# Kernel optimization log

Hardware: AMD Instinct MI355X
Metric: run time of the kernel (lower is better)

Reference implementation:

```python
import jax, jax.numpy as jnp
import numpy as np

B, S, D, EXP = 2, 2048, 128, 16
N = D * EXP  # state_dim = 2048


def setup_inputs() -> dict:
    key = jax.random.key(0)
    ks = jax.random.split(key, 11)
    s_in = 1.0 / np.sqrt(D)   # torch Linear default init bound for dim->N layers
    s_out = 1.0 / np.sqrt(N)  # for out_proj (N->dim)
    x = jax.random.normal(ks[0], (B, S, D), dtype=jnp.float32)
    W_B = jax.random.uniform(ks[1], (N, D), jnp.float32, -s_in, s_in)
    b_B = jax.random.uniform(ks[2], (N,), jnp.float32, -s_in, s_in)
    W_C = jax.random.uniform(ks[3], (N, D), jnp.float32, -s_in, s_in)
    b_C = jax.random.uniform(ks[4], (N,), jnp.float32, -s_in, s_in)
    W_dt = jax.random.uniform(ks[5], (N, D), jnp.float32, -s_in, s_in)
    b_dt = jax.random.uniform(ks[6], (N,), jnp.float32, -s_in, s_in)
    A_log = jnp.log(jax.random.uniform(ks[7], (N,), jnp.float32) * 0.5 + 0.5)
    W_out = jax.random.uniform(ks[8], (D, N), jnp.float32, -s_out, s_out)
    b_out = jax.random.uniform(ks[9], (D,), jnp.float32, -s_out, s_out)
    return {"x": x, "W_B": W_B, "b_B": b_B, "W_C": W_C, "b_C": b_C,
            "W_dt": W_dt, "b_dt": b_dt, "A_log": A_log,
            "W_out": W_out, "b_out": b_out}


def reference(x, W_B, b_B, W_C, b_C, W_dt, b_dt, A_log, W_out, b_out):
    # Featurizer projections: [B,S,D] -> [B,S,N]
    B_feat = jnp.einsum('bsd,nd->bsn', x, W_B) + b_B
    C_feat = jnp.einsum('bsd,nd->bsn', x, W_C) + b_C
    dt = jax.nn.softplus(jnp.einsum('bsd,nd->bsn', x, W_dt) + b_dt)
    A = -jnp.exp(A_log)                # [N]
    A_bar = jnp.exp(dt * A)            # [B,S,N]
    B_bar = dt * B_feat                # [B,S,N]

    # Sequential diagonal scan: h_t = A_t * h_{t-1} + B_t ; y_t = C_t * h_t
    def step(h, abc):
        a_t, b_t, c_t = abc            # each [B,N]
        h = a_t * h + b_t
        return h, c_t * h

    h0 = jnp.zeros((x.shape[0], N), dtype=x.dtype)
    xs = (jnp.swapaxes(A_bar, 0, 1),   # [S,B,N]
          jnp.swapaxes(B_bar, 0, 1),
          jnp.swapaxes(C_feat, 0, 1))
    _, ys = jax.lax.scan(step, h0, xs)  # ys: [S,B,N]
    y = jnp.swapaxes(ys, 0, 1)          # [B,S,N]
    return jnp.einsum('bsn,dn->bsd', y, W_out) + b_out
```

## Files before the change

### kernel.cpp

```cpp
#include <hip/hip_runtime.h>


#define BB 2
#define SS 2048
#define DDIM 128
#define NDIM 2048
#define TT (BB*SS)
#define NTILE (TT/16)

typedef short short8 __attribute__((ext_vector_type(8)));
typedef float floatx4 __attribute__((ext_vector_type(4)));

__device__ __forceinline__ unsigned short f2b(float f){
  unsigned u = __float_as_uint(f);
  u += 0x7FFFu + ((u >> 16) & 1u);
  return (unsigned short)(u >> 16);
}
__device__ __forceinline__ float softplus_f(float v){
  return v > 15.f ? v : __logf(1.f + __expf(v));
}
__device__ __forceinline__ void pack8(const float* __restrict__ s,
                                      unsigned short* __restrict__ d){
  floatx4 v0 = *(const floatx4*)s;
  floatx4 v1 = *(const floatx4*)(s + 4);
  short8 r;
  r[0]=(short)f2b(v0[0]); r[1]=(short)f2b(v0[1]); r[2]=(short)f2b(v0[2]); r[3]=(short)f2b(v0[3]);
  r[4]=(short)f2b(v1[0]); r[5]=(short)f2b(v1[1]); r[6]=(short)f2b(v1[2]); r[7]=(short)f2b(v1[3]);
  *(short8*)d = r;
}

__global__ void prep_kernel(const float* __restrict__ x,
                            const float* __restrict__ W_B,
                            const float* __restrict__ W_C,
                            const float* __restrict__ W_dt,
                            const float* __restrict__ A_log,
                            const float* __restrict__ W_out,
                            unsigned short* __restrict__ xp,
                            unsigned short* __restrict__ Wp3,
                            unsigned short* __restrict__ Wop,
                            float* __restrict__ Aval,
                            unsigned long long* __restrict__ Sbuf){
  const int gid = blockIdx.x * blockDim.x + threadIdx.x;
  if (gid < 32768) Sbuf[gid] = 0ull;
  if (gid < 2048) Aval[gid] = -__expf(A_log[gid]);
  if (gid < 65536){
    int g = gid, tile = g >> 8, kk = (g >> 6) & 3, lane = g & 63;
    int q = lane >> 4, m = lane & 15;
    pack8(x + (size_t)(tile*16 + m)*DDIM + kk*32 + q*8, xp + (size_t)g*8);
  }
  if (gid < 98304){
    int mat = gid >> 15, g = gid & 32767;
    const float* W = (mat == 0) ? W_B : (mat == 1 ? W_dt : W_C);
    int tile = g >> 8, kk = (g >> 6) & 3, lane = g & 63;
    int q = lane >> 4, m = lane & 15;
    pack8(W + (size_t)(tile*16 + m)*DDIM + kk*32 + q*8,
          Wp3 + (size_t)mat*262144 + (size_t)g*8);
  }
  if (gid < 32768){
    int g = gid, tile = g >> 12, kk = (g >> 6) & 63, lane = g & 63;
    int q = lane >> 4, m = lane & 15;
    pack8(W_out + (size_t)(tile*16 + m)*NDIM + kk*32 + q*8, Wop + (size_t)g*8);
  }
}

__global__ __launch_bounds__(256, 2) void projscan_kernel(
    const unsigned short* __restrict__ xp,
    const unsigned short* __restrict__ Wp3,
    const float* __restrict__ b_B,
    const float* __restrict__ b_dt,
    const float* __restrict__ b_C,
    const float* __restrict__ Aval,
    unsigned long long* __restrict__ Sbuf,
    unsigned short* __restrict__ ybp){
  __shared__ unsigned short sW[3*4096];
  __shared__ unsigned short sYT[4][16*40];
  __shared__ float sPw[4][32], sHw[4][32];
  __shared__ float sIw[4][32];
  const int tid  = threadIdx.x;
  const int lane = tid & 63;
  const int wv   = tid >> 6;
  const int m    = lane & 15;
  const int q    = lane >> 4;
  const int p    = blockIdx.y * 16 + blockIdx.x;
  const int xcd  = p & 7;
  const int slot = p >> 3;
  const int rr   = slot & 15;
  const int j    = slot >> 4;
  const int row  = xcd*16 + rr;
  const int by   = row >> 1;
  const int bx   = (row & 1)*8 + j;
  const int n0   = by*32;

  for (int i = tid; i < 1536; i += 256){
    int mat = i >> 9, rem = i & 511;
    *(short8*)(sW + mat*4096 + rem*8) =
        *(const short8*)(Wp3 + (size_t)mat*262144 + (size_t)by*4096 + rem*8);
  }
  __syncthreads();

  float bBv[2], bDv[2], bCv[2], Avv[2];
#pragma unroll
  for (int nt = 0; nt < 2; ++nt){
    const int n = n0 + nt*16 + m;
    bBv[nt] = b_B[n]; bDv[nt] = b_dt[n]; bCv[nt] = b_C[n]; Avv[nt] = Aval[n];
  }

  unsigned ypk[4][2][2], cpk[4][2][2];
  float pe_t[4][2], he_t[4][2];
  float pa_run[2] = {1.f, 1.f}, ha_run[2] = {0.f, 0.f};

#pragma unroll
  for (int i = 0; i < 4; ++i){
    const int tile = bx*16 + wv*4 + i;
    short8 xf[4];
#pragma unroll
    for (int kk = 0; kk < 4; ++kk)
      xf[kk] = *(const short8*)(xp + (size_t)tile*2048 + kk*512 + lane*8);

    floatx4 acc[3][2];
#pragma unroll
    for (int mat = 0; mat < 3; ++mat)
#pragma unroll
      for (int nt = 0; nt < 2; ++nt)
        acc[mat][nt] = (floatx4){0.f,0.f,0.f,0.f};
#pragma unroll
    for (int nt = 0; nt < 2; ++nt)
#pragma unroll
      for (int kk = 0; kk < 4; ++kk){
        short8 wB = *(const short8*)(sW +         nt*2048 + kk*512 + lane*8);
        short8 wD = *(const short8*)(sW + 4096 +  nt*2048 + kk*512 + lane*8);
        short8 wC = *(const short8*)(sW + 8192 +  nt*2048 + kk*512 + lane*8);
        acc[0][nt] = __builtin_amdgcn_mfma_f32_16x16x32_bf16(xf[kk], wB, acc[0][nt], 0, 0, 0);
        acc[1][nt] = __builtin_amdgcn_mfma_f32_16x16x32_bf16(xf[kk], wD, acc[1][nt], 0, 0, 0);
        acc[2][nt] = __builtin_amdgcn_mfma_f32_16x16x32_bf16(xf[kk], wC, acc[2][nt], 0, 0, 0);
      }

#pragma unroll
    for (int nt = 0; nt < 2; ++nt){
      float Ar[4], Br[4], Cc[4];
#pragma unroll
      for (int r = 0; r < 4; ++r){
        float dtv = softplus_f(acc[1][nt][r] + bDv[nt]);
        Ar[r] = __expf(dtv * Avv[nt]);
        Br[r] = dtv * (acc[0][nt][r] + bBv[nt]);
        Cc[r] = acc[2][nt][r] + bCv[nt];
      }
      float P = Ar[0], H = Br[0];
#pragma unroll
      for (int r = 1; r < 4; ++r){ H = Ar[r]*H + Br[r]; P *= Ar[r]; }
      float pp = __shfl(P, (lane - 16) & 63, 64);
      float hh = __shfl(H, (lane - 16) & 63, 64);
      if (q >= 1){ H = P*hh + H; P *= pp; }
      pp = __shfl(P, (lane - 32) & 63, 64);
      hh = __shfl(H, (lane - 32) & 63, 64);
      if (q >= 2){ H = P*hh + H; P *= pp; }
      float pe = __shfl(P, (lane - 16) & 63, 64);
      float he = __shfl(H, (lane - 16) & 63, 64);
      if (q == 0){ pe = 1.f; he = 0.f; }
      float pb = __shfl(P, m + 48, 64);
      float hb = __shfl(H, m + 48, 64);

      float h = he, pa = pe;
      unsigned short yr[4], cr[4];
#pragma unroll
      for (int r = 0; r < 4; ++r){
        h = Ar[r]*h + Br[r];
        pa *= Ar[r];
        yr[r] = f2b(Cc[r]*h);
        cr[r] = f2b(Cc[r]*pa);
      }
      ypk[i][nt][0] = (unsigned)yr[0] | ((unsigned)yr[1] << 16);
      ypk[i][nt][1] = (unsigned)yr[2] | ((unsigned)yr[3] << 16);
      cpk[i][nt][0] = (unsigned)cr[0] | ((unsigned)cr[1] << 16);
      cpk[i][nt][1] = (unsigned)cr[2] | ((unsigned)cr[3] << 16);

      pe_t[i][nt] = pa_run[nt];
      he_t[i][nt] = ha_run[nt];
      ha_run[nt] = pb*ha_run[nt] + hb;
      pa_run[nt] *= pb;
    }
  }
  if (q == 0){
#pragma unroll
    for (int nt = 0; nt < 2; ++nt){
      sPw[wv][nt*16 + m] = pa_run[nt];
      sHw[wv][nt*16 + m] = ha_run[nt];
    }
  }
  __syncthreads();

  if (tid < 32){
    float Pw[4], Hw[4];
#pragma unroll
    for (int w2 = 0; w2 < 4; ++w2){ Pw[w2] = sPw[w2][tid]; Hw[w2] = sHw[w2][tid]; }
    float pb = 1.f, hb = 0.f;
#pragma unroll
    for (int w2 = 0; w2 < 4; ++w2){ hb = Pw[w2]*hb + Hw[w2]; pb *= Pw[w2]; }
    float pbc = fmaxf(pb, 1e-30f);
    __hip_atomic_store(Sbuf + (size_t)(by*16 + bx)*32 + tid,
        ((unsigned long long)__float_as_uint(pbc) << 32) |
         (unsigned long long)__float_as_uint(hb),
        __ATOMIC_RELAXED, __HIP_MEMORY_SCOPE_AGENT);
    float S = 0.f;
    const int cnt = bx & 7;
    if (cnt){
      const int j0 = bx & ~7;
      unsigned long long v0=0,v1=0,v2=0,v3=0,v4=0,v5=0,v6=0;
      unsigned got = 0;
      const unsigned all = (1u << cnt) - 1u;
      const unsigned long long* base = Sbuf + (size_t)(by*16 + j0)*32 + tid;
      for (;;){
#define LOOKBACK(J, V)                                                          \
        if (J < cnt && !(got & (1u << J))){                                     \
          unsigned long long a = __hip_atomic_load(base + (size_t)J*32,         \
              __ATOMIC_RELAXED, __HIP_MEMORY_SCOPE_AGENT);                      \
          if ((unsigned)(a >> 32) != 0u){ V = a; got |= 1u << J; }              \
        }
        LOOKBACK(0, v0) LOOKBACK(1, v1) LOOKBACK(2, v2) LOOKBACK(3, v3)
        LOOKBACK(4, v4) LOOKBACK(5, v5) LOOKBACK(6, v6)
#undef LOOKBACK
        if (got == all) break;
        __builtin_amdgcn_s_sleep(1);
      }
#define COMPOSE(J, V)                                                           \
      if (J < cnt) S = __uint_as_float((unsigned)(V >> 32))*S +                 \
                       __uint_as_float((unsigned)V);
      COMPOSE(0, v0) COMPOSE(1, v1) COMPOSE(2, v2) COMPOSE(3, v3)
      COMPOSE(4, v4) COMPOSE(5, v5) COMPOSE(6, v6)
#undef COMPOSE
    }
    float s = S;
#pragma unroll
    for (int w2 = 0; w2 < 4; ++w2){
      sIw[w2][tid] = s;
      s = Pw[w2]*s + Hw[w2];
    }
  }
  __syncthreads();

  float iw[2];
#pragma unroll
  for (int nt = 0; nt < 2; ++nt) iw[nt] = sIw[wv][nt*16 + m];
#pragma unroll
  for (int i = 0; i < 4; ++i){
    const int tile = bx*16 + wv*4 + i;
#pragma unroll
    for (int nt = 0; nt < 2; ++nt){
      float it = pe_t[i][nt]*iw[nt] + he_t[i][nt];
#pragma unroll
      for (int j2 = 0; j2 < 2; ++j2){
        unsigned yp = ypk[i][nt][j2], cp = cpk[i][nt][j2];
        float y0 = __uint_as_float(yp << 16);
        float y1 = __uint_as_float(yp & 0xffff0000u);
        float c0 = __uint_as_float(cp << 16);
        float c1 = __uint_as_float(cp & 0xffff0000u);
        sYT[wv][(q*4 + j2*2 + 0)*40 + nt*16 + m] = f2b(y0 + c0*it);
        sYT[wv][(q*4 + j2*2 + 1)*40 + nt*16 + m] = f2b(y1 + c1*it);
      }
    }
    short8 yv = *(const short8*)&sYT[wv][m*40 + q*8];
    *(short8*)(ybp + (size_t)tile*32768 + (size_t)by*512 + (size_t)lane*8) = yv;
  }
}

__global__ void outproj_kernel(const unsigned short* __restrict__ ybp,
                               const unsigned short* __restrict__ Wop,
                               const float* __restrict__ b_out,
                               float* __restrict__ out){
  __shared__ float red[4*2048];
  const int tid  = threadIdx.x;
  const int lane = tid & 63;
  const int wv   = tid >> 6;
  const int m    = lane & 15;
  const int q    = lane >> 4;
  const int tile = blockIdx.x;

  floatx4 acc[8];
#pragma unroll
  for (int dt = 0; dt < 8; ++dt) acc[dt] = (floatx4){0.f,0.f,0.f,0.f};

  const unsigned short* aP = ybp + (size_t)tile*32768 + lane*8;
  const unsigned short* bP = Wop + (size_t)lane*8;
#pragma unroll 4
  for (int kk = wv*16; kk < wv*16 + 16; ++kk){
    short8 af = *(const short8*)(aP + (size_t)kk*512);
#pragma unroll
    for (int dt = 0; dt < 8; ++dt){
      short8 bf = *(const short8*)(bP + (size_t)dt*32768 + (size_t)kk*512);
      acc[dt] = __builtin_amdgcn_mfma_f32_16x16x32_bf16(af, bf, acc[dt], 0, 0, 0);
    }
  }
#pragma unroll
  for (int dt = 0; dt < 8; ++dt)
#pragma unroll
    for (int r = 0; r < 4; ++r)
      red[wv*2048 + (q*4 + r)*128 + dt*16 + m] = acc[dt][r];
  __syncthreads();
#pragma unroll
  for (int i = 0; i < 8; ++i){
    int idx = i*256 + tid;
    float s = red[idx] + red[2048 + idx] + red[4096 + idx] + red[6144 + idx];
    int tl = idx >> 7, d = idx & 127;
    out[(size_t)(tile*16 + tl)*DDIM + d] = s + b_out[d];
  }
}

extern "C" void kernel_launch(void* const* d_in, const int* in_sizes, int n_in,
                              void* d_out, int out_size, void* d_ws, size_t ws_size,
                              hipStream_t stream) {
  const float* x     = (const float*)d_in[0];
  const float* W_B   = (const float*)d_in[1];
  const float* b_B   = (const float*)d_in[2];
  const float* W_C   = (const float*)d_in[3];
  const float* b_C   = (const float*)d_in[4];
  const float* W_dt  = (const float*)d_in[5];
  const float* b_dt  = (const float*)d_in[6];
  const float* A_log = (const float*)d_in[7];
  const float* W_out = (const float*)d_in[8];
  const float* b_out = (const float*)d_in[9];
  float* out = (float*)d_out;

  char* w = (char*)d_ws;
  unsigned short* xp    = (unsigned short*)(w + 0x0000000);
  unsigned short* Wp3   = (unsigned short*)(w + 0x0100000);
  unsigned short* Wop   = (unsigned short*)(w + 0x0280000);
  float*          Aval  = (float*)         (w + 0x0300000);
  unsigned short* ybp   = (unsigned short*)(w + 0x0310000);
  unsigned long long* Sbuf = (unsigned long long*)(w + 0x1310000);

  prep_kernel<<<384, 256, 0, stream>>>(
      x, W_B, W_C, W_dt, A_log, W_out, xp, Wp3, Wop, Aval, Sbuf);

  projscan_kernel<<<dim3(16, 64), 256, 0, stream>>>(
      xp, Wp3, b_B, b_dt, b_C, Aval, Sbuf, ybp);

  outproj_kernel<<<NTILE, 256, 0, stream>>>(ybp, Wop, b_out, out);
}
```

Before: 115.5 us.

## Recompute projections after lookback instead of holding scan state in registers

The first pass of the projection-scan kernel now computes only the B and dt projections, enough to form block carries. After the decoupled lookback it recomputes all three projections and the local scan, applies the incoming carry directly, and packs outputs with a hardware bf16 convert instruction. This removes the large per-thread arrays of packed y/c values that were held across the lookback, cutting register pressure at the cost of repeating the MFMA and transcendental work. The change also lengthens the lookback sleep with a backoff, and doubles outproj to 512 threads so each wave handles half as many k-slices, with a larger shared reduction.

Result: slower. 118.3 us (+2.4%).

```diff
diff --git a/kernel.cpp b/kernel.cpp
--- a/kernel.cpp
+++ b/kernel.cpp
@@ -15,6 +15,11 @@
   unsigned u = __float_as_uint(f);
   u += 0x7FFFu + ((u >> 16) & 1u);
   return (unsigned short)(u >> 16);
+}
+__device__ __forceinline__ unsigned cvt_pk_bf16(float lo, float hi){
+  unsigned r;
+  asm("v_cvt_pk_bf16_f32 %0, %1, %2" : "=v"(r) : "v"(lo), "v"(hi));
+  return r;
 }
 __device__ __forceinline__ float softplus_f(float v){
   return v > 15.f ? v : __logf(1.f + __expf(v));
@@ -73,7 +78,7 @@
     unsigned long long* __restrict__ Sbuf,
     unsigned short* __restrict__ ybp){
   __shared__ unsigned short sW[3*4096];
-  __shared__ unsigned short sYT[4][16*40];
+  __shared__ unsigned short sYT[4][640];
   __shared__ float sPw[4][32], sHw[4][32];
   __shared__ float sIw[4][32];
   const int tid  = threadIdx.x;
@@ -105,10 +110,7 @@
     bBv[nt] = b_B[n]; bDv[nt] = b_dt[n]; bCv[nt] = b_C[n]; Avv[nt] = Aval[n];
   }
 
-  unsigned ypk[4][2][2], cpk[4][2][2];
-  float pe_t[4][2], he_t[4][2];
   float pa_run[2] = {1.f, 1.f}, ha_run[2] = {0.f, 0.f};
-
 #pragma unroll
   for (int i = 0; i < 4; ++i){
     const int tile = bx*16 + wv*4 + i;
@@ -117,65 +119,45 @@
     for (int kk = 0; kk < 4; ++kk)
       xf[kk] = *(const short8*)(xp + (size_t)tile*2048 + kk*512 + lane*8);
 
-    floatx4 acc[3][2];
-#pragma unroll
-    for (int mat = 0; mat < 3; ++mat)
-#pragma unroll
-      for (int nt = 0; nt < 2; ++nt)
-        acc[mat][nt] = (floatx4){0.f,0.f,0.f,0.f};
+    floatx4 aB[2], aD[2];
+#pragma unroll
+    for (int nt = 0; nt < 2; ++nt){
+      aB[nt] = (floatx4){0.f,0.f,0.f,0.f};
+      aD[nt] = (floatx4){0.f,0.f,0.f,0.f};
+    }
 #pragma unroll
     for (int nt = 0; nt < 2; ++nt)
 #pragma unroll
       for (int kk = 0; kk < 4; ++kk){
         short8 wB = *(const short8*)(sW +         nt*2048 + kk*512 + lane*8);
         short8 wD = *(const short8*)(sW + 4096 +  nt*2048 + kk*512 + lane*8);
-        short8 wC = *(const short8*)(sW + 8192 +  nt*2048 + kk*512 + lane*8);
-        acc[0][nt] = __builtin_amdgcn_mfma_f32_16x16x32_bf16(xf[kk], wB, acc[0][nt], 0, 0, 0);
-        acc[1][nt] = __builtin_amdgcn_mfma_f32_16x16x32_bf16(xf[kk], wD, acc[1][nt], 0, 0, 0);
-        acc[2][nt] = __builtin_amdgcn_mfma_f32_16x16x32_bf16(xf[kk], wC, acc[2][nt], 0, 0, 0);
+        aB[nt] = __builtin_amdgcn_mfma_f32_16x16x32_bf16(xf[kk], wB, aB[nt], 0, 0, 0);
+        aD[nt] = __builtin_amdgcn_mfma_f32_16x16x32_bf16(xf[kk], wD, aD[nt], 0, 0, 0);
       }
 
 #pragma unroll
     for (int nt = 0; nt < 2; ++nt){
-      float Ar[4], Br[4], Cc[4];
-#pragma unroll
-      for (int r = 0; r < 4; ++r){
-        float dtv = softplus_f(acc[1][nt][r] + bDv[nt]);
-        Ar[r] = __expf(dtv * Avv[nt]);
-        Br[r] = dtv * (acc[0][nt][r] + bBv[nt]);
-        Cc[r] = acc[2][nt][r] + bCv[nt];
-      }
-      float P = Ar[0], H = Br[0];
-#pragma unroll
-      for (int r = 1; r < 4; ++r){ H = Ar[r]*H + Br[r]; P *= Ar[r]; }
+      float P, H;
+      {
+        float Ar[4], Br[4];
+#pragma unroll
+        for (int r = 0; r < 4; ++r){
+          float dtv = softplus_f(aD[nt][r] + bDv[nt]);
+          Ar[r] = __expf(dtv * Avv[nt]);
+          Br[r] = dtv * (aB[nt][r] + bBv[nt]);
+        }
+        P = Ar[0]; H = Br[0];
+#pragma unroll
+        for (int r = 1; r < 4; ++r){ H = Ar[r]*H + Br[r]; P *= Ar[r]; }
+      }
       float pp = __shfl(P, (lane - 16) & 63, 64);
       float hh = __shfl(H, (lane - 16) & 63, 64);
       if (q >= 1){ H = P*hh + H; P *= pp; }
       pp = __shfl(P, (lane - 32) & 63, 64);
       hh = __shfl(H, (lane - 32) & 63, 64);
       if (q >= 2){ H = P*hh + H; P *= pp; }
-      float pe = __shfl(P, (lane - 16) & 63, 64);
-      float he = __shfl(H, (lane - 16) & 63, 64);
-      if (q == 0){ pe = 1.f; he = 0.f; }
       float pb = __shfl(P, m + 48, 64);
       float hb = __shfl(H, m + 48, 64);
-
-      float h = he, pa = pe;
-      unsigned short yr[4], cr[4];
-#pragma unroll
-      for (int r = 0; r < 4; ++r){
-        h = Ar[r]*h + Br[r];
-        pa *= Ar[r];
-        yr[r] = f2b(Cc[r]*h);
-        cr[r] = f2b(Cc[r]*pa);
-      }
-      ypk[i][nt][0] = (unsigned)yr[0] | ((unsigned)yr[1] << 16);
-      ypk[i][nt][1] = (unsigned)yr[2] | ((unsigned)yr[3] << 16);
-      cpk[i][nt][0] = (unsigned)cr[0] | ((unsigned)cr[1] << 16);
-      cpk[i][nt][1] = (unsigned)cr[2] | ((unsigned)cr[3] << 16);
-
-      pe_t[i][nt] = pa_run[nt];
-      he_t[i][nt] = ha_run[nt];
       ha_run[nt] = pb*ha_run[nt] + hb;
       pa_run[nt] *= pb;
     }
@@ -207,6 +189,7 @@
       const int j0 = bx & ~7;
       unsigned long long v0=0,v1=0,v2=0,v3=0,v4=0,v5=0,v6=0;
       unsigned got = 0;
+      int spin = 0;
       const unsigned all = (1u << cnt) - 1u;
       const unsigned long long* base = Sbuf + (size_t)(by*16 + j0)*32 + tid;
       for (;;){
@@ -220,7 +203,9 @@
         LOOKBACK(4, v4) LOOKBACK(5, v5) LOOKBACK(6, v6)
 #undef LOOKBACK
         if (got == all) break;
-        __builtin_amdgcn_s_sleep(1);
+        if (spin < 4) __builtin_amdgcn_s_sleep(2);
+        else          __builtin_amdgcn_s_sleep(8);
+        ++spin;
       }
 #define COMPOSE(J, V)                                                           \
       if (J < cnt) S = __uint_as_float((unsigned)(V >> 32))*S +                 \
@@ -238,36 +223,88 @@
   }
   __syncthreads();
 
-  float iw[2];
-#pragma unroll
-  for (int nt = 0; nt < 2; ++nt) iw[nt] = sIw[wv][nt*16 + m];
+  float it_run[2];
+#pragma unroll
+  for (int nt = 0; nt < 2; ++nt) it_run[nt] = sIw[wv][nt*16 + m];
+
 #pragma unroll
   for (int i = 0; i < 4; ++i){
     const int tile = bx*16 + wv*4 + i;
+    short8 xf[4];
+#pragma unroll
+    for (int kk = 0; kk < 4; ++kk)
+      xf[kk] = *(const short8*)(xp + (size_t)tile*2048 + kk*512 + lane*8);
+
+    floatx4 acc[3][2];
+#pragma unroll
+    for (int mat = 0; mat < 3; ++mat)
+#pragma unroll
+      for (int nt = 0; nt < 2; ++nt)
+        acc[mat][nt] = (floatx4){0.f,0.f,0.f,0.f};
+#pragma unroll
+    for (int nt = 0; nt < 2; ++nt)
+#pragma unroll
+      for (int kk = 0; kk < 4; ++kk){
+        short8 wB = *(const short8*)(sW +         nt*2048 + kk*512 + lane*8);
+        short8 wD = *(const short8*)(sW + 4096 +  nt*2048 + kk*512 + lane*8);
+        short8 wC = *(const short8*)(sW + 8192 +  nt*2048 + kk*512 + lane*8);
+        acc[0][nt] = __builtin_amdgcn_mfma_f32_16x16x32_bf16(xf[kk], wB, acc[0][nt], 0, 0, 0);
+        acc[1][nt] = __builtin_amdgcn_mfma_f32_16x16x32_bf16(xf[kk], wD, acc[1][nt], 0, 0, 0);
+        acc[2][nt] = __builtin_amdgcn_mfma_f32_16x16x32_bf16(xf[kk], wC, acc[2][nt], 0, 0, 0);
+      }
+
 #pragma unroll
     for (int nt = 0; nt < 2; ++nt){
-      float it = pe_t[i][nt]*iw[nt] + he_t[i][nt];
-#pragma unroll
-      for (int j2 = 0; j2 < 2; ++j2){
-        unsigned yp = ypk[i][nt][j2], cp = cpk[i][nt][j2];
-        float y0 = __uint_as_float(yp << 16);
-        float y1 = __uint_as_float(yp & 0xffff0000u);
-        float c0 = __uint_as_float(cp << 16);
-        float c1 = __uint_as_float(cp & 0xffff0000u);
-        sYT[wv][(q*4 + j2*2 + 0)*40 + nt*16 + m] = f2b(y0 + c0*it);
-        sYT[wv][(q*4 + j2*2 + 1)*40 + nt*16 + m] = f2b(y1 + c1*it);
-      }
+      float Ar[4], Br[4], Cc[4];
+#pragma unroll
+      for (int r = 0; r < 4; ++r){
+        float dtv = softplus_f(acc[1][nt][r] + bDv[nt]);
+        Ar[r] = __expf(dtv * Avv[nt]);
+        Br[r] = dtv * (acc[0][nt][r] + bBv[nt]);
+        Cc[r] = acc[2][nt][r] + bCv[nt];
+      }
+      float P = Ar[0], H = Br[0];
+#pragma unroll
+      for (int r = 1; r < 4; ++r){ H = Ar[r]*H + Br[r]; P *= Ar[r]; }
+      float pp = __shfl(P, (lane - 16) & 63, 64);
+      float hh = __shfl(H, (lane - 16) & 63, 64);
+      if (q >= 1){ H = P*hh + H; P *= pp; }
+      pp = __shfl(P, (lane - 32) & 63, 64);
+      hh = __shfl(H, (lane - 32) & 63, 64);
+      if (q >= 2){ H = P*hh + H; P *= pp; }
+      float pe = __shfl(P, (lane - 16) & 63, 64);
+      float he = __shfl(H, (lane - 16) & 63, 64);
+      if (q == 0){ pe = 1.f; he = 0.f; }
+      float pb = __shfl(P, m + 48, 64);
+      float hb = __shfl(H, m + 48, 64);
+
+      float h = pe*it_run[nt] + he;
+      float ys[4];
+#pragma unroll
+      for (int r = 0; r < 4; ++r){
+        h = Ar[r]*h + Br[r];
+        ys[r] = Cc[r]*h;
+      }
+      unsigned y01 = cvt_pk_bf16(ys[0], ys[1]);
+      unsigned y23 = cvt_pk_bf16(ys[2], ys[3]);
+      sYT[wv][(q*4 + 0)*40 + nt*16 + m] = (unsigned short)(y01);
+      sYT[wv][(q*4 + 1)*40 + nt*16 + m] = (unsigned short)(y01 >> 16);
+      sYT[wv][(q*4 + 2)*40 + nt*16 + m] = (unsigned short)(y23);
+      sYT[wv][(q*4 + 3)*40 + nt*16 + m] = (unsigned short)(y23 >> 16);
+
+      it_run[nt] = pb*it_run[nt] + hb;
     }
     short8 yv = *(const short8*)&sYT[wv][m*40 + q*8];
     *(short8*)(ybp + (size_t)tile*32768 + (size_t)by*512 + (size_t)lane*8) = yv;
   }
 }
 
-__global__ void outproj_kernel(const unsigned short* __restrict__ ybp,
-                               const unsigned short* __restrict__ Wop,
-                               const float* __restrict__ b_out,
-                               float* __restrict__ out){
-  __shared__ float red[4*2048];
+__global__ __launch_bounds__(512, 1) void outproj_kernel(
+    const unsigned short* __restrict__ ybp,
+    const unsigned short* __restrict__ Wop,
+    const float* __restrict__ b_out,
+    float* __restrict__ out){
+  __shared__ float red[8*2048];
   const int tid  = threadIdx.x;
   const int lane = tid & 63;
   const int wv   = tid >> 6;
@@ -281,8 +318,8 @@
 
   const unsigned short* aP = ybp + (size_t)tile*32768 + lane*8;
   const unsigned short* bP = Wop + (size_t)lane*8;
-#pragma unroll 4
-  for (int kk = wv*16; kk < wv*16 + 16; ++kk){
+#pragma unroll
+  for (int kk = wv*8; kk < wv*8 + 8; ++kk){
     short8 af = *(const short8*)(aP + (size_t)kk*512);
 #pragma unroll
     for (int dt = 0; dt < 8; ++dt){
@@ -297,9 +334,10 @@
       red[wv*2048 + (q*4 + r)*128 + dt*16 + m] = acc[dt][r];
   __syncthreads();
 #pragma unroll
-  for (int i = 0; i < 8; ++i){
-    int idx = i*256 + tid;
-    float s = red[idx] + red[2048 + idx] + red[4096 + idx] + red[6144 + idx];
+  for (int i = 0; i < 4; ++i){
+    int idx = i*512 + tid;
+    float s = red[idx]          + red[2048 + idx] + red[4096 + idx] + red[6144 + idx]
+            + red[8192 + idx]   + red[10240 + idx] + red[12288 + idx] + red[14336 + idx];
     int tl = idx >> 7, d = idx & 127;
     out[(size_t)(tile*16 + tl)*DDIM + d] = s + b_out[d];
   }
@@ -334,5 +372,5 @@
   projscan_kernel<<<dim3(16, 64), 256, 0, stream>>>(
       xp, Wp3, b_B, b_dt, b_C, Aval, Sbuf, ybp);
 
-  outproj_kernel<<<NTILE, 256, 0, stream>>>(ybp, Wop, b_out, out);
-}
+  outproj_kernel<<<NTILE, 512, 0, stream>>>(ybp, Wop, b_out, out);
+}
```
